# Performance work log

Measured on AMD Instinct MI355X. Metric: run time of the kernel, lower is better.

## Reference

```python
import jax, jax.numpy as jnp
import numpy as np

B, N, D_IN, D_OUT = 16, 2048, 256, 256

def setup_inputs() -> dict:
    key = jax.random.key(0)
    k1, k2, k3 = jax.random.split(key, 3)
    nodes_rep = jax.random.normal(k1, (B, N, D_IN), dtype=jnp.float32)
    adj_metric = jax.random.uniform(k2, (B, N, N), dtype=jnp.float32)
    # xavier_uniform for [D_IN, D_OUT]
    limit = float(np.sqrt(6.0 / (D_IN + D_OUT)))
    attn_weight = jax.random.uniform(k3, (D_IN, D_OUT), dtype=jnp.float32, minval=-limit, maxval=limit)
    attn_bias = jnp.zeros((D_OUT,), dtype=jnp.float32)
    return {"nodes_rep": nodes_rep, "adj_metric": adj_metric,
            "attn_weight": attn_weight, "attn_bias": attn_bias}

def reference(nodes_rep, adj_metric, attn_weight, attn_bias):
    # h: [B, N, D_OUT]
    h = jnp.einsum('bni,io->bno', nodes_rep, attn_weight)
    # scores: [B, N, N]
    scores = jnp.einsum('bno,bmo->bnm', h, h)
    scores = jax.nn.leaky_relu(scores, negative_slope=0.2)
    scores = scores * adj_metric
    attn = jax.nn.softmax(scores, axis=-1)
    # output aggregates the UNtransformed input, then adds bias
    out = jnp.einsum('bnm,bmd->bnd', attn, nodes_rep) + attn_bias
    return out
```

## Files before the change

### kernel.cpp

```cpp
#include <hip/hip_runtime.h>
#include <math.h>
#include <stdint.h>

typedef _Float16 half8 __attribute__((ext_vector_type(8)));
typedef _Float16 half2v __attribute__((ext_vector_type(2)));
typedef float    f32x4 __attribute__((ext_vector_type(4)));
typedef unsigned int uint4v __attribute__((ext_vector_type(4)));

constexpr int Bc = 16, Nn = 2048, Dd = 256;
constexpr int QTI = 64;
constexpr int MC  = 32;

__device__ _Float16 g_Wt[Dd * Dd];

__device__ __forceinline__ void gload16(const void* g, void* l) {
    __builtin_amdgcn_global_load_lds(
        (const __attribute__((address_space(1))) void*)g,
        (__attribute__((address_space(3))) void*)l, 16, 0, 0);
}

__global__ void __launch_bounds__(256)
wt_transpose_kernel(const float* __restrict__ W) {
    __shared__ float ts[64][65];
    const int t = threadIdx.x;
    const int r0 = blockIdx.x * 64;
    const int c0 = blockIdx.y * 64;
    for (int idx = t; idx < 64 * 64; idx += 256) {
        const int i = idx >> 6, j = idx & 63;
        ts[i][j] = W[(r0 + i) * Dd + c0 + j];
    }
    __syncthreads();
    for (int idx = t; idx < 64 * 64; idx += 256) {
        const int c = idx >> 6, rl = idx & 63;
        g_Wt[(c0 + c) * Dd + r0 + rl] = (_Float16)ts[rl][c];
    }
}

__global__ void __launch_bounds__(256, 2)
hgemm_vt_kernel(const float* __restrict__ nodes, _Float16* __restrict__ h16,
                _Float16* __restrict__ vt) {
    __shared__ __align__(16) char lds_raw[67584];
    _Float16 (*Wt_s)[264] = (_Float16 (*)[264])lds_raw;
    _Float16* ts = (_Float16*)lds_raw;

    const int t = threadIdx.x, w = t >> 6, lane = t & 63;
    const int quad = lane >> 4, l16 = lane & 15;
    const size_t row0 = (size_t)blockIdx.x * 64 + 16 * w;

    half8 aq[8];
    {
        const float* src = nodes + (row0 + l16) * Dd + quad * 8;
        #pragma unroll
        for (int kf = 0; kf < 8; ++kf) {
            const f32x4 a0 = *(const f32x4*)(src + kf * 32);
            const f32x4 a1 = *(const f32x4*)(src + kf * 32 + 4);
            half8 a;
            a[0] = (_Float16)a0[0]; a[1] = (_Float16)a0[1];
            a[2] = (_Float16)a0[2]; a[3] = (_Float16)a0[3];
            a[4] = (_Float16)a1[0]; a[5] = (_Float16)a1[1];
            a[6] = (_Float16)a1[2]; a[7] = (_Float16)a1[3];
            aq[kf] = a;
        }
    }
    f32x4 acc[16];
    #pragma unroll
    for (int ot = 0; ot < 16; ++ot) acc[ot] = (f32x4){0.f, 0.f, 0.f, 0.f};

    #pragma unroll
    for (int hh = 0; hh < 2; ++hh) {
        if (hh) __syncthreads();
        #pragma unroll
        for (int ii = 0; ii < 16; ++ii) {
            const int i = t + ii * 256;
            *(half8*)&Wt_s[i >> 5][(i & 31) * 8] =
                *(const half8*)&g_Wt[(size_t)(hh * 128 + (i >> 5)) * Dd + (i & 31) * 8];
        }
        __syncthreads();
        #pragma unroll
        for (int kf = 0; kf < 8; ++kf)
            #pragma unroll
            for (int ot = 0; ot < 8; ++ot) {
                const half8 bw = *(const half8*)&Wt_s[ot * 16 + l16][kf * 32 + quad * 8];
                acc[hh * 8 + ot] = __builtin_amdgcn_mfma_f32_16x16x32_f16(aq[kf], bw, acc[hh * 8 + ot], 0, 0, 0);
            }
    }
    #pragma unroll
    for (int idx = 0; idx < 16; ++idx) {
        const int hh = idx >> 3, ot = idx & 7;
        #pragma unroll
        for (int r = 0; r < 4; ++r)
            h16[(row0 + quad * 4 + r) * Dd + hh * 128 + ot * 16 + l16] = (_Float16)acc[idx][r];
    }

    __syncthreads();
    const int n_local = 16 * w + l16;
    #pragma unroll
    for (int kf = 0; kf < 8; ++kf)
        #pragma unroll
        for (int j = 0; j < 8; ++j) {
            const int d = kf * 32 + quad * 8 + j;
            const int col = (((n_local >> 3) ^ ((d >> 3) & 7)) * 8) + (n_local & 7);
            ts[d * 64 + col] = aq[kf][j];
        }
    __syncthreads();
    const int b  = (int)(((size_t)blockIdx.x * 64) >> 11);
    const int nb = (int)(((size_t)blockIdx.x * 64) & 2047);
    _Float16* vdst = vt + (size_t)b * Dd * Nn;
    #pragma unroll
    for (int ii = 0; ii < 8; ++ii) {
        const int i = t + ii * 256;
        const int d = i >> 3, g = i & 7;
        const int pg = g ^ ((d >> 3) & 7);
        const half8 v = *(const half8*)(ts + d * 64 + pg * 8);
        *(half8*)(vdst + (size_t)d * Nn + nb + g * 8) = v;
    }
}

__global__ void __launch_bounds__(256, 2)
gat_attn_kernel(const _Float16* __restrict__ h, const _Float16* __restrict__ vt,
                const float* __restrict__ adj, const float* __restrict__ bias,
                float* __restrict__ out) {
    __shared__ __align__(16) char lds_raw[65536];
    _Float16* hmA = (_Float16*)lds_raw;
    _Float16* hmB = (_Float16*)(lds_raw + 16384);
    _Float16* vA  = (_Float16*)(lds_raw + 32768);
    _Float16* vB  = (_Float16*)(lds_raw + 49152);
    auto tw = (float (*)[16][69])lds_raw;

    const int t = threadIdx.x, w = t >> 6, lane = t & 63;
    const int quad = lane >> 4, l16 = lane & 15;
    const int b  = blockIdx.x & 15;
    const int q0 = (blockIdx.x >> 4) * QTI;

    const _Float16* hb = h   + (size_t)b * Nn * Dd;
    const _Float16* vb = vt  + (size_t)b * Dd * Nn;
    const float*   abq = adj + ((size_t)b * Nn + (q0 + 16 * w + l16)) * Nn;

    auto STAGE = [&](int mb, _Float16* hmX, _Float16* vX) {
        #pragma unroll
        for (int ii = 0; ii < 4; ++ii) {
            const int i = t + ii * 256;
            const int mp = i >> 5, s = i & 31;
            gload16(hb + (size_t)(mb + mp) * Dd + ((s ^ (mp & 7)) * 8), hmX + i * 8);
        }
        #pragma unroll
        for (int ii = 0; ii < 4; ++ii) {
            const int i = t + ii * 256;
            const int r = i >> 3, pg = i & 7;
            const int g = pg ^ (r & 7);
            gload16(vb + (size_t)(2 * r + (g >> 2)) * Nn + mb + (g & 3) * 8, vX + i * 8);
        }
    };

    STAGE(0, hmA, vA);
    f32x4 adjA[2], adjB[2];
    #pragma unroll
    for (int mt = 0; mt < 2; ++mt)
        adjA[mt] = *(const f32x4*)(abq + mt * 16 + quad * 4);

    half8 bq[8];
    {
        const _Float16* s = hb + (size_t)(q0 + 16 * w + l16) * Dd + quad * 8;
        #pragma unroll
        for (int kf = 0; kf < 8; ++kf) bq[kf] = *(const half8*)(s + kf * 32);
    }

    f32x4 ot_[16];
    #pragma unroll
    for (int dt = 0; dt < 16; ++dt) ot_[dt] = (f32x4){0.f, 0.f, 0.f, 0.f};
    float m_run = -1e30f, l_run = 0.f;

    const int s0 = ((lane >> 4) & 1) * 32 + l16;
    const int s1 = s0 + 16;
    const bool qlow = lane < 32;

    __syncthreads();

    auto CHUNK = [&](int mb, const _Float16* hmC, const _Float16* vC,
                     _Float16* hmN, _Float16* vN,
                     const f32x4 (&ac)[2], f32x4 (&an)[2]) {
        const int mb2 = mb + MC;
        if (mb2 < Nn) {
            STAGE(mb2, hmN, vN);
            #pragma unroll
            for (int mt = 0; mt < 2; ++mt)
                an[mt] = *(const f32x4*)(abq + mb2 + mt * 16 + quad * 4);
        }

        f32x4 st[2];
        st[0] = (f32x4){0.f, 0.f, 0.f, 0.f};
        st[1] = (f32x4){0.f, 0.f, 0.f, 0.f};
        __builtin_amdgcn_s_setprio(1);
        #pragma unroll
        for (int kf = 0; kf < 8; ++kf)
            #pragma unroll
            for (int mt = 0; mt < 2; ++mt) {
                const int m  = mt * 16 + l16;
                const int pg = (kf * 4 + quad) ^ (m & 7);
                const half8 am = *(const half8*)(hmC + m * 256 + pg * 8);
                st[mt] = __builtin_amdgcn_mfma_f32_16x16x32_f16(am, bq[kf], st[mt], 0, 0, 0);
            }
        __builtin_amdgcn_s_setprio(0);

        float rm = -1e30f;
        #pragma unroll
        for (int mt = 0; mt < 2; ++mt)
            #pragma unroll
            for (int r = 0; r < 4; ++r) {
                float s = st[mt][r];
                s = (s >= 0.f) ? s : 0.2f * s;
                s *= ac[mt][r];
                st[mt][r] = s;
                rm = fmaxf(rm, s);
            }
        rm = fmaxf(rm, __shfl_xor(rm, 16));
        rm = fmaxf(rm, __shfl_xor(rm, 32));
        if (!__all(rm <= m_run)) {
            const float mn    = fmaxf(m_run, rm);
            const float alpha = __expf(m_run - mn);
            m_run = mn;
            l_run *= alpha;
            #pragma unroll
            for (int dt = 0; dt < 16; ++dt) {
                ot_[dt][0] *= alpha; ot_[dt][1] *= alpha;
                ot_[dt][2] *= alpha; ot_[dt][3] *= alpha;
            }
        }
        float rs = 0.f;
        #pragma unroll
        for (int mt = 0; mt < 2; ++mt)
            #pragma unroll
            for (int r = 0; r < 4; ++r) {
                const float p = __expf(st[mt][r] - m_run);
                st[mt][r] = p;
                rs += p;
            }
        rs += __shfl_xor(rs, 16);
        rs += __shfl_xor(rs, 32);
        l_run += rs;

        uint32_t pk[2][2];
        #pragma unroll
        for (int mt = 0; mt < 2; ++mt) {
            half2v h01, h23;
            h01[0] = (_Float16)st[mt][0]; h01[1] = (_Float16)st[mt][1];
            h23[0] = (_Float16)st[mt][2]; h23[1] = (_Float16)st[mt][3];
            pk[mt][0] = __builtin_bit_cast(uint32_t, h01);
            pk[mt][1] = __builtin_bit_cast(uint32_t, h23);
        }
        uint4v bw_;
        {
            const uint32_t a00 = (uint32_t)__shfl((int)pk[0][0], s0);
            const uint32_t b00 = (uint32_t)__shfl((int)pk[1][0], s0);
            const uint32_t a10 = (uint32_t)__shfl((int)pk[0][1], s0);
            const uint32_t b10 = (uint32_t)__shfl((int)pk[1][1], s0);
            const uint32_t a01 = (uint32_t)__shfl((int)pk[0][0], s1);
            const uint32_t b01 = (uint32_t)__shfl((int)pk[1][0], s1);
            const uint32_t a11 = (uint32_t)__shfl((int)pk[0][1], s1);
            const uint32_t b11 = (uint32_t)__shfl((int)pk[1][1], s1);
            bw_[0] = qlow ? a00 : b00;
            bw_[1] = qlow ? a10 : b10;
            bw_[2] = qlow ? a01 : b01;
            bw_[3] = qlow ? a11 : b11;
        }
        const half8 bp = __builtin_bit_cast(half8, bw_);

        __builtin_amdgcn_s_setprio(1);
        #pragma unroll
        for (int dt = 0; dt < 16; ++dt) {
            const int d  = dt * 16 + l16;
            const int rp = d >> 1;
            const int gq = ((d & 1) * 4 + quad) ^ (rp & 7);
            const half8 va = *(const half8*)(vC + rp * 64 + gq * 8);
            ot_[dt] = __builtin_amdgcn_mfma_f32_16x16x32_f16(va, bp, ot_[dt], 0, 0, 0);
        }
        __builtin_amdgcn_s_setprio(0);

        __syncthreads();
    };

    for (int mb = 0; mb < Nn; mb += 2 * MC) {
        CHUNK(mb,      hmA, vA, hmB, vB, adjA, adjB);
        CHUNK(mb + MC, hmB, vB, hmA, vA, adjB, adjA);
    }

    __syncthreads();
    const float invl = 1.f / l_run;
    #pragma unroll
    for (int dt = 0; dt < 16; ++dt) {
        ot_[dt][0] *= invl; ot_[dt][1] *= invl;
        ot_[dt][2] *= invl; ot_[dt][3] *= invl;
    }
    float* T = &tw[w][0][0];
    const int rr = lane >> 2, cg = lane & 3;
    float* orow = out + ((size_t)b * Nn + q0 + 16 * w + rr) * Dd;
    #pragma unroll
    for (int dc = 0; dc < 4; ++dc) {
        #pragma unroll
        for (int k4 = 0; k4 < 4; ++k4)
            #pragma unroll
            for (int r = 0; r < 4; ++r)
                T[l16 * 69 + k4 * 16 + quad * 4 + r] = ot_[dc * 4 + k4][r];
        asm volatile("s_waitcnt lgkmcnt(0)" ::: "memory");
        #pragma unroll
        for (int c = 0; c < 4; ++c) {
            f32x4 v;
            #pragma unroll
            for (int e = 0; e < 4; ++e) v[e] = T[rr * 69 + cg * 16 + 4 * c + e];
            const int d = dc * 64 + cg * 16 + 4 * c;
            const f32x4 bs = *(const f32x4*)(bias + d);
            v[0] += bs[0]; v[1] += bs[1]; v[2] += bs[2]; v[3] += bs[3];
            *(f32x4*)(orow + d) = v;
        }
        asm volatile("s_waitcnt lgkmcnt(0)" ::: "memory");
    }
}

extern "C" void kernel_launch(void* const* d_in, const int* in_sizes, int n_in,
                              void* d_out, int out_size, void* d_ws, size_t ws_size,
                              hipStream_t stream) {
    const float* nodes = (const float*)d_in[0];
    const float* adj   = (const float*)d_in[1];
    const float* W     = (const float*)d_in[2];
    const float* bias  = (const float*)d_in[3];
    float* out = (float*)d_out;

    _Float16* h16 = (_Float16*)d_ws;
    _Float16* vtp = h16 + (size_t)Bc * Nn * Dd;

    hipLaunchKernelGGL(wt_transpose_kernel, dim3(4, 4), dim3(256), 0, stream, W);
    hipLaunchKernelGGL(hgemm_vt_kernel, dim3(512), dim3(256), 0, stream, nodes, h16, vtp);
    hipLaunchKernelGGL(gat_attn_kernel, dim3(512), dim3(256), 0, stream, h16, vtp, adj, bias, out);
}
```

Before: 471.4 us.

## Process two query row-tiles per wave with half the waves per block

The attention kernel now launches 128 threads (2 waves) per block, and each wave handles 32 query rows as two 16-row tiles. Every K/V fragment read from LDS then feeds two MFMAs, which halves LDS read traffic per unit of math. In exchange, register pressure roughly doubles (two sets of accumulators and query fragments), occupancy drops to launch_bounds(128,1), and each block has fewer waves to hide latency.

```diff
diff --git a/kernel.cpp b/kernel.cpp
--- a/kernel.cpp
+++ b/kernel.cpp
@@ -116,7 +116,7 @@
     }
 }
 
-__global__ void __launch_bounds__(256, 2)
+__global__ void __launch_bounds__(128, 1)
 gat_attn_kernel(const _Float16* __restrict__ h, const _Float16* __restrict__ vt,
                 const float* __restrict__ adj, const float* __restrict__ bias,
                 float* __restrict__ out) {
@@ -134,18 +134,19 @@
 
     const _Float16* hb = h   + (size_t)b * Nn * Dd;
     const _Float16* vb = vt  + (size_t)b * Dd * Nn;
-    const float*   abq = adj + ((size_t)b * Nn + (q0 + 16 * w + l16)) * Nn;
+    const float* abq0 = adj + ((size_t)b * Nn + (q0 + 32 * w + l16)) * Nn;
+    const float* abq1 = abq0 + (size_t)16 * Nn;
 
     auto STAGE = [&](int mb, _Float16* hmX, _Float16* vX) {
         #pragma unroll
-        for (int ii = 0; ii < 4; ++ii) {
-            const int i = t + ii * 256;
+        for (int ii = 0; ii < 8; ++ii) {
+            const int i = t + ii * 128;
             const int mp = i >> 5, s = i & 31;
             gload16(hb + (size_t)(mb + mp) * Dd + ((s ^ (mp & 7)) * 8), hmX + i * 8);
         }
         #pragma unroll
-        for (int ii = 0; ii < 4; ++ii) {
-            const int i = t + ii * 256;
+        for (int ii = 0; ii < 8; ++ii) {
+            const int i = t + ii * 128;
             const int r = i >> 3, pg = i & 7;
             const int g = pg ^ (r & 7);
             gload16(vb + (size_t)(2 * r + (g >> 2)) * Nn + mb + (g & 3) * 8, vX + i * 8);
@@ -153,22 +154,30 @@
     };
 
     STAGE(0, hmA, vA);
-    f32x4 adjA[2], adjB[2];
-    #pragma unroll
-    for (int mt = 0; mt < 2; ++mt)
-        adjA[mt] = *(const f32x4*)(abq + mt * 16 + quad * 4);
-
-    half8 bq[8];
+    f32x4 adjA0[2], adjA1[2], adjB0[2], adjB1[2];
+    #pragma unroll
+    for (int mt = 0; mt < 2; ++mt) {
+        adjA0[mt] = *(const f32x4*)(abq0 + mt * 16 + quad * 4);
+        adjA1[mt] = *(const f32x4*)(abq1 + mt * 16 + quad * 4);
+    }
+
+    half8 bq0[8], bq1[8];
     {
-        const _Float16* s = hb + (size_t)(q0 + 16 * w + l16) * Dd + quad * 8;
-        #pragma unroll
-        for (int kf = 0; kf < 8; ++kf) bq[kf] = *(const half8*)(s + kf * 32);
-    }
-
-    f32x4 ot_[16];
-    #pragma unroll
-    for (int dt = 0; dt < 16; ++dt) ot_[dt] = (f32x4){0.f, 0.f, 0.f, 0.f};
-    float m_run = -1e30f, l_run = 0.f;
+        const _Float16* s = hb + (size_t)(q0 + 32 * w + l16) * Dd + quad * 8;
+        #pragma unroll
+        for (int kf = 0; kf < 8; ++kf) {
+            bq0[kf] = *(const half8*)(s + kf * 32);
+            bq1[kf] = *(const half8*)(s + 16 * Dd + kf * 32);
+        }
+    }
+
+    f32x4 o0[16], o1[16];
+    #pragma unroll
+    for (int dt = 0; dt < 16; ++dt) {
+        o0[dt] = (f32x4){0.f, 0.f, 0.f, 0.f};
+        o1[dt] = (f32x4){0.f, 0.f, 0.f, 0.f};
+    }
+    float m0 = -1e30f, l0 = 0.f, m1 = -1e30f, l1 = 0.f;
 
     const int s0 = ((lane >> 4) & 1) * 32 + l16;
     const int s1 = s0 + 16;
@@ -176,32 +185,8 @@
 
     __syncthreads();
 
-    auto CHUNK = [&](int mb, const _Float16* hmC, const _Float16* vC,
-                     _Float16* hmN, _Float16* vN,
-                     const f32x4 (&ac)[2], f32x4 (&an)[2]) {
-        const int mb2 = mb + MC;
-        if (mb2 < Nn) {
-            STAGE(mb2, hmN, vN);
-            #pragma unroll
-            for (int mt = 0; mt < 2; ++mt)
-                an[mt] = *(const f32x4*)(abq + mb2 + mt * 16 + quad * 4);
-        }
-
-        f32x4 st[2];
-        st[0] = (f32x4){0.f, 0.f, 0.f, 0.f};
-        st[1] = (f32x4){0.f, 0.f, 0.f, 0.f};
-        __builtin_amdgcn_s_setprio(1);
-        #pragma unroll
-        for (int kf = 0; kf < 8; ++kf)
-            #pragma unroll
-            for (int mt = 0; mt < 2; ++mt) {
-                const int m  = mt * 16 + l16;
-                const int pg = (kf * 4 + quad) ^ (m & 7);
-                const half8 am = *(const half8*)(hmC + m * 256 + pg * 8);
-                st[mt] = __builtin_amdgcn_mfma_f32_16x16x32_f16(am, bq[kf], st[mt], 0, 0, 0);
-            }
-        __builtin_amdgcn_s_setprio(0);
-
+    auto SM = [&](f32x4 (&st)[2], const f32x4 (&ac)[2], float& mr, float& lr,
+                  f32x4 (&o)[16], uint32_t (&pk)[2][2]) {
         float rm = -1e30f;
         #pragma unroll
         for (int mt = 0; mt < 2; ++mt)
@@ -215,15 +200,15 @@
             }
         rm = fmaxf(rm, __shfl_xor(rm, 16));
         rm = fmaxf(rm, __shfl_xor(rm, 32));
-        if (!__all(rm <= m_run)) {
-            const float mn    = fmaxf(m_run, rm);
-            const float alpha = __expf(m_run - mn);
-            m_run = mn;
-            l_run *= alpha;
+        if (!__all(rm <= mr)) {
+            const float mn    = fmaxf(mr, rm);
+            const float alpha = __expf(mr - mn);
+            mr = mn;
+            lr *= alpha;
             #pragma unroll
             for (int dt = 0; dt < 16; ++dt) {
-                ot_[dt][0] *= alpha; ot_[dt][1] *= alpha;
-                ot_[dt][2] *= alpha; ot_[dt][3] *= alpha;
+                o[dt][0] *= alpha; o[dt][1] *= alpha;
+                o[dt][2] *= alpha; o[dt][3] *= alpha;
             }
         }
         float rs = 0.f;
@@ -231,15 +216,13 @@
         for (int mt = 0; mt < 2; ++mt)
             #pragma unroll
             for (int r = 0; r < 4; ++r) {
-                const float p = __expf(st[mt][r] - m_run);
+                const float p = __expf(st[mt][r] - mr);
                 st[mt][r] = p;
                 rs += p;
             }
         rs += __shfl_xor(rs, 16);
         rs += __shfl_xor(rs, 32);
-        l_run += rs;
-
-        uint32_t pk[2][2];
+        lr += rs;
         #pragma unroll
         for (int mt = 0; mt < 2; ++mt) {
             half2v h01, h23;
@@ -248,22 +231,59 @@
             pk[mt][0] = __builtin_bit_cast(uint32_t, h01);
             pk[mt][1] = __builtin_bit_cast(uint32_t, h23);
         }
+    };
+    auto REDIST = [&](const uint32_t (&pk)[2][2]) -> half8 {
         uint4v bw_;
-        {
-            const uint32_t a00 = (uint32_t)__shfl((int)pk[0][0], s0);
-            const uint32_t b00 = (uint32_t)__shfl((int)pk[1][0], s0);
-            const uint32_t a10 = (uint32_t)__shfl((int)pk[0][1], s0);
-            const uint32_t b10 = (uint32_t)__shfl((int)pk[1][1], s0);
-            const uint32_t a01 = (uint32_t)__shfl((int)pk[0][0], s1);
-            const uint32_t b01 = (uint32_t)__shfl((int)pk[1][0], s1);
-            const uint32_t a11 = (uint32_t)__shfl((int)pk[0][1], s1);
-            const uint32_t b11 = (uint32_t)__shfl((int)pk[1][1], s1);
-            bw_[0] = qlow ? a00 : b00;
-            bw_[1] = qlow ? a10 : b10;
-            bw_[2] = qlow ? a01 : b01;
-            bw_[3] = qlow ? a11 : b11;
-        }
-        const half8 bp = __builtin_bit_cast(half8, bw_);
+        const uint32_t a00 = (uint32_t)__shfl((int)pk[0][0], s0);
+        const uint32_t b00 = (uint32_t)__shfl((int)pk[1][0], s0);
+        const uint32_t a10 = (uint32_t)__shfl((int)pk[0][1], s0);
+        const uint32_t b10 = (uint32_t)__shfl((int)pk[1][1], s0);
+        const uint32_t a01 = (uint32_t)__shfl((int)pk[0][0], s1);
+        const uint32_t b01 = (uint32_t)__shfl((int)pk[1][0], s1);
+        const uint32_t a11 = (uint32_t)__shfl((int)pk[0][1], s1);
+        const uint32_t b11 = (uint32_t)__shfl((int)pk[1][1], s1);
+        bw_[0] = qlow ? a00 : b00;
+        bw_[1] = qlow ? a10 : b10;
+        bw_[2] = qlow ? a01 : b01;
+        bw_[3] = qlow ? a11 : b11;
+        return __builtin_bit_cast(half8, bw_);
+    };
+
+    auto CHUNK = [&](int mb, const _Float16* hmC, const _Float16* vC,
+                     _Float16* hmN, _Float16* vN,
+                     const f32x4 (&ac0)[2], const f32x4 (&ac1)[2],
+                     f32x4 (&an0)[2], f32x4 (&an1)[2]) {
+        const int mb2 = mb + MC;
+        if (mb2 < Nn) {
+            STAGE(mb2, hmN, vN);
+            #pragma unroll
+            for (int mt = 0; mt < 2; ++mt) {
+                an0[mt] = *(const f32x4*)(abq0 + mb2 + mt * 16 + quad * 4);
+                an1[mt] = *(const f32x4*)(abq1 + mb2 + mt * 16 + quad * 4);
+            }
+        }
+
+        f32x4 st0[2], st1[2];
+        st0[0] = (f32x4){0.f, 0.f, 0.f, 0.f}; st0[1] = st0[0];
+        st1[0] = st0[0];                       st1[1] = st0[0];
+        __builtin_amdgcn_s_setprio(1);
+        #pragma unroll
+        for (int kf = 0; kf < 8; ++kf)
+            #pragma unroll
+            for (int mt = 0; mt < 2; ++mt) {
+                const int m  = mt * 16 + l16;
+                const int pg = (kf * 4 + quad) ^ (m & 7);
+                const half8 am = *(const half8*)(hmC + m * 256 + pg * 8);
+                st0[mt] = __builtin_amdgcn_mfma_f32_16x16x32_f16(am, bq0[kf], st0[mt], 0, 0, 0);
+                st1[mt] = __builtin_amdgcn_mfma_f32_16x16x32_f16(am, bq1[kf], st1[mt], 0, 0, 0);
+            }
+        __builtin_amdgcn_s_setprio(0);
+
+        uint32_t pk0[2][2], pk1[2][2];
+        SM(st0, ac0, m0, l0, o0, pk0);
+        SM(st1, ac1, m1, l1, o1, pk1);
+        const half8 bp0 = REDIST(pk0);
+        const half8 bp1 = REDIST(pk1);
 
         __builtin_amdgcn_s_setprio(1);
         #pragma unroll
@@ -272,7 +292,8 @@
             const int rp = d >> 1;
             const int gq = ((d & 1) * 4 + quad) ^ (rp & 7);
             const half8 va = *(const half8*)(vC + rp * 64 + gq * 8);
-            ot_[dt] = __builtin_amdgcn_mfma_f32_16x16x32_f16(va, bp, ot_[dt], 0, 0, 0);
+            o0[dt] = __builtin_amdgcn_mfma_f32_16x16x32_f16(va, bp0, o0[dt], 0, 0, 0);
+            o1[dt] = __builtin_amdgcn_mfma_f32_16x16x32_f16(va, bp1, o1[dt], 0, 0, 0);
         }
         __builtin_amdgcn_s_setprio(0);
 
@@ -280,40 +301,44 @@
     };
 
     for (int mb = 0; mb < Nn; mb += 2 * MC) {
-        CHUNK(mb,      hmA, vA, hmB, vB, adjA, adjB);
-        CHUNK(mb + MC, hmB, vB, hmA, vA, adjB, adjA);
-    }
-
-    __syncthreads();
-    const float invl = 1.f / l_run;
-    #pragma unroll
-    for (int dt = 0; dt < 16; ++dt) {
-        ot_[dt][0] *= invl; ot_[dt][1] *= invl;
-        ot_[dt][2] *= invl; ot_[dt][3] *= invl;
-    }
-    float* T = &tw[w][0][0];
-    const int rr = lane >> 2, cg = lane & 3;
-    float* orow = out + ((size_t)b * Nn + q0 + 16 * w + rr) * Dd;
-    #pragma unroll
-    for (int dc = 0; dc < 4; ++dc) {
-        #pragma unroll
-        for (int k4 = 0; k4 < 4; ++k4)
-            #pragma unroll
-            for (int r = 0; r < 4; ++r)
-                T[l16 * 69 + k4 * 16 + quad * 4 + r] = ot_[dc * 4 + k4][r];
-        asm volatile("s_waitcnt lgkmcnt(0)" ::: "memory");
-        #pragma unroll
-        for (int c = 0; c < 4; ++c) {
-            f32x4 v;
-            #pragma unroll
-            for (int e = 0; e < 4; ++e) v[e] = T[rr * 69 + cg * 16 + 4 * c + e];
-            const int d = dc * 64 + cg * 16 + 4 * c;
-            const f32x4 bs = *(const f32x4*)(bias + d);
-            v[0] += bs[0]; v[1] += bs[1]; v[2] += bs[2]; v[3] += bs[3];
-            *(f32x4*)(orow + d) = v;
-        }
-        asm volatile("s_waitcnt lgkmcnt(0)" ::: "memory");
-    }
+        CHUNK(mb,      hmA, vA, hmB, vB, adjA0, adjA1, adjB0, adjB1);
+        CHUNK(mb + MC, hmB, vB, hmA, vA, adjB0, adjB1, adjA0, adjA1);
+    }
+
+    __syncthreads();
+    auto EPI = [&](f32x4 (&o)[16], float lr, int qrow) {
+        const float invl = 1.f / lr;
+        #pragma unroll
+        for (int dt = 0; dt < 16; ++dt) {
+            o[dt][0] *= invl; o[dt][1] *= invl;
+            o[dt][2] *= invl; o[dt][3] *= invl;
+        }
+        float* T = &tw[w][0][0];
+        const int rr = lane >> 2, cg = lane & 3;
+        float* orow = out + ((size_t)b * Nn + qrow + rr) * Dd;
+        #pragma unroll
+        for (int dc = 0; dc < 4; ++dc) {
+            #pragma unroll
+            for (int k4 = 0; k4 < 4; ++k4)
+                #pragma unroll
+                for (int r = 0; r < 4; ++r)
+                    T[l16 * 69 + k4 * 16 + quad * 4 + r] = o[dc * 4 + k4][r];
+            asm volatile("s_waitcnt lgkmcnt(0)" ::: "memory");
+            #pragma unroll
+            for (int c = 0; c < 4; ++c) {
+                f32x4 v;
+                #pragma unroll
+                for (int e = 0; e < 4; ++e) v[e] = T[rr * 69 + cg * 16 + 4 * c + e];
+                const int d = dc * 64 + cg * 16 + 4 * c;
+                const f32x4 bs = *(const f32x4*)(bias + d);
+                v[0] += bs[0]; v[1] += bs[1]; v[2] += bs[2]; v[3] += bs[3];
+                *(f32x4*)(orow + d) = v;
+            }
+            asm volatile("s_waitcnt lgkmcnt(0)" ::: "memory");
+        }
+    };
+    EPI(o0, l0, q0 + 32 * w);
+    EPI(o1, l1, q0 + 32 * w + 16);
 }
 
 extern "C" void kernel_launch(void* const* d_in, const int* in_sizes, int n_in,
@@ -330,5 +355,5 @@
 
     hipLaunchKernelGGL(wt_transpose_kernel, dim3(4, 4), dim3(256), 0, stream, W);
     hipLaunchKernelGGL(hgemm_vt_kernel, dim3(512), dim3(256), 0, stream, nodes, h16, vtp);
-    hipLaunchKernelGGL(gat_attn_kernel, dim3(512), dim3(256), 0, stream, h16, vtp, adj, bias, out);
-}
+    hipLaunchKernelGGL(gat_attn_kernel, dim3(512), dim3(128), 0, stream, h16, vtp, adj, bias, out);
+}
```

After: 502.7 us. +6.6%, slower.
